# Kernel optimization log

Measured on AMD Instinct MI355X. Metric: run time of the kernel, lower is better.

The kernel has to match this reference:

```python
import jax, jax.numpy as jnp
import numpy as np

R = 8          # n attention heads / input capsules (config_spin['r'])
U2 = 1024      # 2 * d_lstm
DA = 512       # d_a
SC = 128       # n_seen_class
OA = 16        # output_atoms
NR = 3         # n_routing
B = 128
T = 256


def setup_inputs() -> dict:
    key = jax.random.key(0)
    k1, k2, k3, k4 = jax.random.split(key, 4)
    x = jax.random.normal(k1, (B, T, U2), jnp.float32)              # encoder output outp
    WS1 = jax.random.normal(k2, (R, DA, U2), jnp.float32) * 0.03    # r stacked Linear(2u->d_a) weights
    WS2 = jax.random.normal(k3, (R, U2, DA), jnp.float32) * 0.03    # r stacked Linear(d_a->2u) weights
    capsule_weights = jax.random.normal(k4, (R, U2, SC * OA), jnp.float32) * 0.03
    return {"x": x, "WS1": WS1, "WS2": WS2, "capsule_weights": capsule_weights}


def _squash(s):
    # s: [B, out_dim, atoms]; squash along atoms (dim=2 in torch)
    norm = jnp.linalg.norm(s, axis=2, keepdims=True)
    n2 = norm * norm
    return s / norm * (n2 / (1.0 + n2))


def reference(x, WS1, WS2, capsule_weights):
    # --- encoder_dim_att: r-head structured self-attention ---
    hbar = jax.nn.relu(jnp.einsum('btu,rau->brta', x, WS1))          # [B,r,T,d_a]
    scores = jnp.einsum('brta,rua->brtu', hbar, WS2)                 # [B,r,T,2u]
    alphas = jax.nn.softmax(scores, axis=2)                          # softmax over seq (torch dim=1)
    m = jnp.einsum('brtu,btu->bru', alphas, x)                       # sentence_embedding [B,r,2u]

    # --- votes: tiled multiply+sum == contraction over input_atoms ---
    votes = jnp.einsum('bru,ruo->bro', m, capsule_weights)           # [B,r,SC*OA]
    votes = votes.reshape(B, R, SC, OA)                              # [B,r,SC,OA]

    # --- dynamic routing ---
    logits0 = jnp.zeros((B, R, SC), x.dtype)

    def step(logits, _):
        route = jax.nn.softmax(logits, axis=2)                       # [B,r,SC]
        preact = jnp.einsum('brc,brco->bco', route, votes)           # [B,SC,OA]
        act = _squash(preact)                                        # [B,SC,OA]
        dist = jnp.einsum('brco,bco->brc', votes, act)               # agreement [B,r,SC]
        return logits + dist, act

    _, acts = jax.lax.scan(step, logits0, None, length=NR)
    activation = acts[-1]                                            # last-iteration activation
    return jnp.linalg.norm(activation, axis=-1)                      # class logits [B,SC]
```

## Files before the change

### kernel.cpp

```cpp
#include <hip/hip_runtime.h>


typedef __attribute__((ext_vector_type(8))) short bf16x8;
typedef __attribute__((ext_vector_type(8))) unsigned short u16x8;
typedef __attribute__((ext_vector_type(4))) float f32x4;

#define LDT 40

__device__ __forceinline__ unsigned short f2bf(float f) {
    unsigned u = __float_as_uint(f);
    u += 0x7FFF + ((u >> 16) & 1);
    return (unsigned short)(u >> 16);
}
__device__ __forceinline__ float bf2f(unsigned short h) {
    return __uint_as_float(((unsigned)h) << 16);
}

typedef __attribute__((address_space(1))) void gvoid;
typedef __attribute__((address_space(3))) void lvoid;
__device__ __forceinline__ void gll16(const unsigned short* g, unsigned short* l) {
    __builtin_amdgcn_global_load_lds((gvoid*)g, (lvoid*)l, 16, 0, 0);
}

__global__ __launch_bounds__(256) void k0_hi(const float* __restrict__ src,
                                             unsigned short* __restrict__ hi,
                                             int n4) {
    int i = blockIdx.x * 256 + threadIdx.x;
    if (i >= n4) return;
    float4 v = ((const float4*)src)[i];
    ushort4 h;
    h.x = f2bf(v.x); h.y = f2bf(v.y); h.z = f2bf(v.z); h.w = f2bf(v.w);
    ((ushort4*)hi)[i] = h;
}

__global__ __launch_bounds__(256) void k0_tsplit(const float* __restrict__ cw,
                                                 unsigned short* __restrict__ ch,
                                                 unsigned short* __restrict__ cl) {
    __shared__ unsigned short Th[64 * 68], Tl[64 * 68];
    const int tid = threadIdx.x;
    const int n0 = blockIdx.x * 64, k0 = blockIdx.y * 64, r = blockIdx.z;
    const float* src = cw + (size_t)r * 1024 * 2048;
#pragma unroll
    for (int p = 0; p < 4; p++) {
        const int kl = p * 16 + (tid >> 4);
        const int nl = (tid & 15) * 4;
        float4 v = *(const float4*)(src + (size_t)(k0 + kl) * 2048 + n0 + nl);
        float vv[4] = {v.x, v.y, v.z, v.w};
#pragma unroll
        for (int e = 0; e < 4; e++) {
            unsigned short h = f2bf(vv[e]);
            Th[(nl + e) * 68 + kl] = h;
            Tl[(nl + e) * 68 + kl] = f2bf(vv[e] - bf2f(h));
        }
    }
    __syncthreads();
    const int nl = tid >> 2, kl = (tid & 3) * 16;
    unsigned short* dh = ch + ((size_t)r * 2048 + n0 + nl) * 1024 + k0 + kl;
    unsigned short* dl = cl + ((size_t)r * 2048 + n0 + nl) * 1024 + k0 + kl;
    *(u16x8*)(dh)     = *(const u16x8*)&Th[nl * 68 + kl];
    *(u16x8*)(dh + 8) = *(const u16x8*)&Th[nl * 68 + kl + 8];
    *(u16x8*)(dl)     = *(const u16x8*)&Tl[nl * 68 + kl];
    *(u16x8*)(dl + 8) = *(const u16x8*)&Tl[nl * 68 + kl + 8];
}

__global__ __launch_bounds__(256) void k1_all(
    const unsigned short* __restrict__ Xb,
    const unsigned short* __restrict__ W1h,
    unsigned short* __restrict__ HhA) {
    __shared__ __align__(16) unsigned short Ah[2][128 * 32];
    __shared__ __align__(16) unsigned short Bh[2][128 * 32];
    const int tid = threadIdx.x;
    const int m0 = blockIdx.x * 128, n0 = blockIdx.y * 128, r = blockIdx.z;
    const int wave = tid >> 6, lane = tid & 63;
    const int wm = (wave >> 1) * 64, wn = (wave & 1) * 64;
    const int lx = lane & 15, qd = lane >> 4;
    const int rl = lane >> 2, cl = (lane & 3) * 8;

    f32x4 acc[4][4];
#pragma unroll
    for (int i = 0; i < 4; i++)
#pragma unroll
        for (int j = 0; j < 4; j++) acc[i][j] = (f32x4){0.f, 0.f, 0.f, 0.f};

    const unsigned short* asrc = Xb + (size_t)(m0 + rl) * 1024 + cl;
    const unsigned short* bsrc =
        W1h + (size_t)r * 512 * 1024 + (size_t)(n0 + rl) * 1024 + cl;

#define K1_STAGE(AD, BD, KK)                                         \
    do {                                                             \
        _Pragma("unroll") for (int s = 0; s < 2; s++) {              \
            const int c = wave * 2 + s;                              \
            gll16(asrc + (size_t)c * 16 * 1024 + (KK), (AD) + c * 512); \
            gll16(bsrc + (size_t)c * 16 * 1024 + (KK), (BD) + c * 512); \
        }                                                            \
    } while (0)

    K1_STAGE(Ah[0], Bh[0], 0);
    __syncthreads();
    int p = 0;
    for (int t = 0; t < 32; ++t) {
        if (t < 31) K1_STAGE(Ah[p ^ 1], Bh[p ^ 1], (t + 1) * 32);
        const unsigned short* Ab = Ah[p];
        const unsigned short* Bb = Bh[p];
        bf16x8 fa[4], fb[4];
#pragma unroll
        for (int i = 0; i < 4; i++) {
            fa[i] = *(const bf16x8*)&Ab[(wm + 16 * i + lx) * 32 + 8 * qd];
            fb[i] = *(const bf16x8*)&Bb[(wn + 16 * i + lx) * 32 + 8 * qd];
        }
#pragma unroll
        for (int i = 0; i < 4; i++)
#pragma unroll
            for (int j = 0; j < 4; j++)
                acc[i][j] = __builtin_amdgcn_mfma_f32_16x16x32_bf16(fa[i], fb[j], acc[i][j], 0, 0, 0);
        __syncthreads();
        p ^= 1;
    }
#undef K1_STAGE

    unsigned short* Hh = HhA + (size_t)r * 8192 * 512;
#pragma unroll
    for (int i = 0; i < 4; i++)
#pragma unroll
        for (int j = 0; j < 4; j++) {
            const int col = n0 + wn + 16 * j + lx;
#pragma unroll
            for (int p2 = 0; p2 < 4; p2++) {
                const int row = m0 + wm + 16 * i + 4 * qd + p2;
                Hh[(size_t)row * 512 + col] = f2bf(fmaxf(acc[i][j][p2], 0.f));
            }
        }
}

template <int XBF>
__global__ __launch_bounds__(256) void k1_hbar_mfma(
    const void* __restrict__ Xv,
    const unsigned short* __restrict__ Wh,
    unsigned short* __restrict__ Hh) {
    __shared__ unsigned short Ah[128 * LDT];
    __shared__ unsigned short Bh[128 * LDT];
    const int tid = threadIdx.x;
    const int m0 = blockIdx.x * 128, n0 = blockIdx.y * 128;
    const int wave = tid >> 6, lane = tid & 63;
    const int wm = (wave >> 1) * 64, wn = (wave & 1) * 64;
    const int lx = lane & 15, qd = lane >> 4;
    const int srow = tid >> 1, scol = (tid & 1) * 16;

    f32x4 acc[4][4];
#pragma unroll
    for (int i = 0; i < 4; i++)
#pragma unroll
        for (int j = 0; j < 4; j++) acc[i][j] = (f32x4){0.f, 0.f, 0.f, 0.f};

    const unsigned short* whrow = Wh + (size_t)(n0 + srow) * 1024 + scol;
    unsigned short* ah = &Ah[srow * LDT + scol];
    unsigned short* bh = &Bh[srow * LDT + scol];

    for (int k0 = 0; k0 < 1024; k0 += 32) {
        if (XBF) {
            const unsigned short* xrow =
                (const unsigned short*)Xv + (size_t)(m0 + srow) * 1024 + scol;
            u16x8 a0 = *(const u16x8*)(xrow + k0);
            u16x8 a1 = *(const u16x8*)(xrow + k0 + 8);
            *(u16x8*)(ah) = a0; *(u16x8*)(ah + 8) = a1;
        } else {
            const float* xrow = (const float*)Xv + (size_t)(m0 + srow) * 1024 + scol;
            float4 v0 = *(const float4*)(xrow + k0);
            float4 v1 = *(const float4*)(xrow + k0 + 4);
            float4 v2 = *(const float4*)(xrow + k0 + 8);
            float4 v3 = *(const float4*)(xrow + k0 + 12);
            float vv[16] = {v0.x, v0.y, v0.z, v0.w, v1.x, v1.y, v1.z, v1.w,
                            v2.x, v2.y, v2.z, v2.w, v3.x, v3.y, v3.z, v3.w};
            u16x8 p0, p1;
#pragma unroll
            for (int e = 0; e < 8; e++) p0[e] = f2bf(vv[e]);
#pragma unroll
            for (int e = 0; e < 8; e++) p1[e] = f2bf(vv[8 + e]);
            *(u16x8*)(ah) = p0; *(u16x8*)(ah + 8) = p1;
        }
        u16x8 b0 = *(const u16x8*)(whrow + k0);
        u16x8 b1 = *(const u16x8*)(whrow + k0 + 8);
        *(u16x8*)(bh) = b0; *(u16x8*)(bh + 8) = b1;
        __syncthreads();

        bf16x8 fa[4], fb[4];
#pragma unroll
        for (int i = 0; i < 4; i++) {
            fa[i] = *(const bf16x8*)&Ah[(wm + 16 * i + lx) * LDT + 8 * qd];
            fb[i] = *(const bf16x8*)&Bh[(wn + 16 * i + lx) * LDT + 8 * qd];
        }
#pragma unroll
        for (int i = 0; i < 4; i++)
#pragma unroll
            for (int j = 0; j < 4; j++)
                acc[i][j] = __builtin_amdgcn_mfma_f32_16x16x32_bf16(fa[i], fb[j], acc[i][j], 0, 0, 0);
        __syncthreads();
    }

#pragma unroll
    for (int i = 0; i < 4; i++)
#pragma unroll
        for (int j = 0; j < 4; j++) {
            const int col = n0 + wn + 16 * j + lx;
#pragma unroll
            for (int p = 0; p < 4; p++) {
                const int row = m0 + wm + 16 * i + 4 * qd + p;
                Hh[(size_t)row * 512 + col] = f2bf(fmaxf(acc[i][j][p], 0.f));
            }
        }
}

__global__ __launch_bounds__(256) void k2_allr(
    const unsigned short* __restrict__ HhA,
    const unsigned short* __restrict__ W2h,
    const float* __restrict__ x, float* __restrict__ m_out, int b0) {
    __shared__ __align__(16) unsigned short Ah[2][256 * 32];
    __shared__ __align__(16) unsigned short Bh[2][64 * 32];
    __shared__ float mred[256], sred[256], pred[256];
    const int tid = threadIdx.x;
    const int b_local = blockIdx.x, b = b0 + b_local;
    const int u0 = blockIdx.y * 64;
    const int r_base = blockIdx.z * 4;
    const int wave = tid >> 6, lane = tid & 63;
    const int lx = lane & 15, qd = lane >> 4;
    const int rl = lane >> 2, cl = (lane & 3) * 8;
    const int ub = wave * 16 + rl;
    const int uperm = 4 * (ub & 15) + (ub >> 4);

    for (int rr = 0; rr < 4; ++rr) {
        const int r = r_base + rr;
        const unsigned short* asrc =
            HhA + (size_t)r * 8192 * 512 + (size_t)(b_local * 256 + rl) * 512 + cl;
        const unsigned short* bsrc =
            W2h + (size_t)r * 1024 * 512 + (size_t)(u0 + uperm) * 512 + cl;

        f32x4 acc[4][4];
#pragma unroll
        for (int i = 0; i < 4; i++)
#pragma unroll
            for (int j = 0; j < 4; j++) acc[i][j] = (f32x4){0.f, 0.f, 0.f, 0.f};

#define K2_STAGE(AD, BD, KK)                                            \
    do {                                                                \
        _Pragma("unroll") for (int s = 0; s < 4; s++) {                 \
            const int c = wave * 4 + s;                                 \
            gll16(asrc + (size_t)c * 16 * 512 + (KK), (AD) + c * 512);  \
        }                                                               \
        gll16(bsrc + (KK), (BD) + wave * 512);                          \
    } while (0)

        K2_STAGE(Ah[0], Bh[0], 0);
        __syncthreads();
        int p = 0;
        for (int t = 0; t < 16; ++t) {
            if (t < 15) K2_STAGE(Ah[p ^ 1], Bh[p ^ 1], (t + 1) * 32);
            const unsigned short* Ab = Ah[p];
            const unsigned short* Bb = Bh[p];
            bf16x8 fa[4], fb[4];
#pragma unroll
            for (int i = 0; i < 4; i++) {
                fa[i] = *(const bf16x8*)&Ab[(64 * wave + 16 * i + lx) * 32 + 8 * qd];
                fb[i] = *(const bf16x8*)&Bb[(16 * i + lx) * 32 + 8 * qd];
            }
#pragma unroll
            for (int i = 0; i < 4; i++)
#pragma unroll
                for (int j = 0; j < 4; j++)
                    acc[i][j] = __builtin_amdgcn_mfma_f32_16x16x32_bf16(fa[i], fb[j], acc[i][j], 0, 0, 0);
            __syncthreads();
            p ^= 1;
        }
#undef K2_STAGE

        float cm[4];
#pragma unroll
        for (int j = 0; j < 4; j++) {
            float mx = acc[0][j][0];
#pragma unroll
            for (int i = 0; i < 4; i++)
#pragma unroll
                for (int p2 = 0; p2 < 4; p2++) mx = fmaxf(mx, acc[i][j][p2]);
            mx = fmaxf(mx, __shfl_xor(mx, 16, 64));
            mx = fmaxf(mx, __shfl_xor(mx, 32, 64));
            if (qd == 0) mred[wave * 64 + 16 * j + lx] = mx;
        }
        __syncthreads();
#pragma unroll
        for (int j = 0; j < 4; j++) {
            const int c = 16 * j + lx;
            cm[j] = fmaxf(fmaxf(mred[c], mred[64 + c]),
                          fmaxf(mred[128 + c], mred[192 + c]));
        }

        float ds[4] = {0.f, 0.f, 0.f, 0.f}, pm[4] = {0.f, 0.f, 0.f, 0.f};
        const float* xb = x + (size_t)b * 256 * 1024 + u0 + 4 * lx;
#pragma unroll
        for (int i = 0; i < 4; i++) {
#pragma unroll
            for (int p2 = 0; p2 < 4; p2++) {
                const int t = 64 * wave + 16 * i + 4 * qd + p2;
                float4 xv = *(const float4*)(xb + (size_t)t * 1024);
                float xa[4] = {xv.x, xv.y, xv.z, xv.w};
#pragma unroll
                for (int j = 0; j < 4; j++) {
                    float e = __expf(acc[i][j][p2] - cm[j]);
                    ds[j] += e;
                    pm[j] += e * xa[j];
                }
            }
        }
#pragma unroll
        for (int j = 0; j < 4; j++) {
            ds[j] += __shfl_xor(ds[j], 16, 64);
            ds[j] += __shfl_xor(ds[j], 32, 64);
            pm[j] += __shfl_xor(pm[j], 16, 64);
            pm[j] += __shfl_xor(pm[j], 32, 64);
            if (qd == 0) {
                sred[wave * 64 + 16 * j + lx] = ds[j];
                pred[wave * 64 + 16 * j + lx] = pm[j];
            }
        }
        __syncthreads();
        if (tid < 64) {
            float dsum = sred[tid] + sred[64 + tid] + sred[128 + tid] + sred[192 + tid];
            float psum = pred[tid] + pred[64 + tid] + pred[128 + tid] + pred[192 + tid];
            const int u = u0 + 4 * (tid & 15) + (tid >> 4);
            m_out[(size_t)(r * 128 + b) * 1024 + u] = psum / dsum;
        }
        __syncthreads();
    }
}

__global__ __launch_bounds__(256) void k2_mfma(
    const unsigned short* __restrict__ Hh,
    const unsigned short* __restrict__ W2h,
    const float* __restrict__ x, float* __restrict__ m_out, int b0, int r) {
    __shared__ __align__(16) unsigned short Ah[256 * 32];
    __shared__ __align__(16) unsigned short Bh[64 * 32];
    __shared__ float mred[256], sred[256], pred[256];
    const int tid = threadIdx.x;
    const int b_local = blockIdx.x, b = b0 + b_local;
    const int u0 = blockIdx.y * 64;
    const int wave = tid >> 6, lane = tid & 63;
    const int lx = lane & 15, qd = lane >> 4;
    const int rl = lane >> 2, cl = (lane & 3) * 8;

    f32x4 acc[4][4];
#pragma unroll
    for (int i = 0; i < 4; i++)
#pragma unroll
        for (int j = 0; j < 4; j++) acc[i][j] = (f32x4){0.f, 0.f, 0.f, 0.f};

    const unsigned short* asrc = Hh + (size_t)(b_local * 256 + rl) * 512 + cl;
    const int ub = wave * 16 + rl;
    const unsigned short* bsrc =
        W2h + (size_t)(u0 + 4 * (ub & 15) + (ub >> 4)) * 512 + cl;

    for (int k0 = 0; k0 < 512; k0 += 32) {
#pragma unroll
        for (int s = 0; s < 4; s++) {
            const int c = wave * 4 + s;
            gll16(asrc + (size_t)c * 16 * 512 + k0, &Ah[c * 512]);
        }
        gll16(bsrc + k0, &Bh[wave * 512]);
        __syncthreads();
        bf16x8 fa[4], fb[4];
#pragma unroll
        for (int i = 0; i < 4; i++) {
            fa[i] = *(const bf16x8*)&Ah[(64 * wave + 16 * i + lx) * 32 + 8 * qd];
            fb[i] = *(const bf16x8*)&Bh[(16 * i + lx) * 32 + 8 * qd];
        }
#pragma unroll
        for (int i = 0; i < 4; i++)
#pragma unroll
            for (int j = 0; j < 4; j++)
                acc[i][j] = __builtin_amdgcn_mfma_f32_16x16x32_bf16(fa[i], fb[j], acc[i][j], 0, 0, 0);
        __syncthreads();
    }

    float cm[4];
#pragma unroll
    for (int j = 0; j < 4; j++) {
        float mx = acc[0][j][0];
#pragma unroll
        for (int i = 0; i < 4; i++)
#pragma unroll
            for (int p = 0; p < 4; p++) mx = fmaxf(mx, acc[i][j][p]);
        mx = fmaxf(mx, __shfl_xor(mx, 16, 64));
        mx = fmaxf(mx, __shfl_xor(mx, 32, 64));
        if (qd == 0) mred[wave * 64 + 16 * j + lx] = mx;
    }
    __syncthreads();
#pragma unroll
    for (int j = 0; j < 4; j++) {
        const int c = 16 * j + lx;
        cm[j] = fmaxf(fmaxf(mred[c], mred[64 + c]), fmaxf(mred[128 + c], mred[192 + c]));
    }

    float ds[4] = {0.f, 0.f, 0.f, 0.f}, pm[4] = {0.f, 0.f, 0.f, 0.f};
    const float* xb = x + (size_t)b * 256 * 1024 + u0 + 4 * lx;
#pragma unroll
    for (int i = 0; i < 4; i++) {
#pragma unroll
        for (int p = 0; p < 4; p++) {
            const int t = 64 * wave + 16 * i + 4 * qd + p;
            float4 xv = *(const float4*)(xb + (size_t)t * 1024);
            float xa[4] = {xv.x, xv.y, xv.z, xv.w};
#pragma unroll
            for (int j = 0; j < 4; j++) {
                float e = __expf(acc[i][j][p] - cm[j]);
                ds[j] += e;
                pm[j] += e * xa[j];
            }
        }
    }
#pragma unroll
    for (int j = 0; j < 4; j++) {
        ds[j] += __shfl_xor(ds[j], 16, 64);
        ds[j] += __shfl_xor(ds[j], 32, 64);
        pm[j] += __shfl_xor(pm[j], 16, 64);
        pm[j] += __shfl_xor(pm[j], 32, 64);
        if (qd == 0) {
            sred[wave * 64 + 16 * j + lx] = ds[j];
            pred[wave * 64 + 16 * j + lx] = pm[j];
        }
    }
    __syncthreads();
    if (tid < 64) {
        float dsum = sred[tid] + sred[64 + tid] + sred[128 + tid] + sred[192 + tid];
        float psum = pred[tid] + pred[64 + tid] + pred[128 + tid] + pred[192 + tid];
        const int u = u0 + 4 * (tid & 15) + (tid >> 4);
        m_out[(size_t)(r * 128 + b) * 1024 + u] = psum / dsum;
    }
}

__global__ __launch_bounds__(256) void k3_votes_mfma(
    const float* __restrict__ Mb,
    const unsigned short* __restrict__ CWh,
    const unsigned short* __restrict__ CWl,
    float* __restrict__ V) {
    __shared__ unsigned short Ah[128 * LDT];
    __shared__ unsigned short Bh[64 * LDT], Bl[64 * LDT];
    const int tid = threadIdx.x;
    const int r = blockIdx.x, n0 = blockIdx.y * 64;
    const int wave = tid >> 6, lane = tid & 63;
    const int wr = wave >> 1, wc = wave & 1;
    const int lx = lane & 15, qd = lane >> 4;
    const int srow = tid >> 1, scol = (tid & 1) * 16;
    const int brow = tid >> 2, bcol = (tid & 3) * 8;

    const float* arow = Mb + (size_t)(r * 128 + srow) * 1024 + scol;
    const unsigned short* bhrow = CWh + ((size_t)r * 2048 + n0 + brow) * 1024 + bcol;
    const unsigned short* blrow = CWl + ((size_t)r * 2048 + n0 + brow) * 1024 + bcol;

    f32x4 acc[4][2];
#pragma unroll
    for (int i = 0; i < 4; i++)
#pragma unroll
        for (int j = 0; j < 2; j++) acc[i][j] = (f32x4){0.f, 0.f, 0.f, 0.f};

    for (int k0 = 0; k0 < 1024; k0 += 32) {
        float4 v0 = *(const float4*)(arow + k0);
        float4 v1 = *(const float4*)(arow + k0 + 4);
        float4 v2 = *(const float4*)(arow + k0 + 8);
        float4 v3 = *(const float4*)(arow + k0 + 12);
        float vv[16] = {v0.x, v0.y, v0.z, v0.w, v1.x, v1.y, v1.z, v1.w,
                        v2.x, v2.y, v2.z, v2.w, v3.x, v3.y, v3.z, v3.w};
        u16x8 p0, p1;
#pragma unroll
        for (int e = 0; e < 8; e++) p0[e] = f2bf(vv[e]);
#pragma unroll
        for (int e = 0; e < 8; e++) p1[e] = f2bf(vv[8 + e]);
        *(u16x8*)&Ah[srow * LDT + scol] = p0;
        *(u16x8*)&Ah[srow * LDT + scol + 8] = p1;
        *(u16x8*)&Bh[brow * LDT + bcol] = *(const u16x8*)(bhrow + k0);
        *(u16x8*)&Bl[brow * LDT + bcol] = *(const u16x8*)(blrow + k0);
        __syncthreads();

        bf16x8 fa[4], fbh[2], fbl[2];
#pragma unroll
        for (int i = 0; i < 4; i++)
            fa[i] = *(const bf16x8*)&Ah[(64 * wr + 16 * i + lx) * LDT + 8 * qd];
#pragma unroll
        for (int j = 0; j < 2; j++) {
            fbh[j] = *(const bf16x8*)&Bh[(32 * wc + 16 * j + lx) * LDT + 8 * qd];
            fbl[j] = *(const bf16x8*)&Bl[(32 * wc + 16 * j + lx) * LDT + 8 * qd];
        }
#pragma unroll
        for (int i = 0; i < 4; i++)
#pragma unroll
            for (int j = 0; j < 2; j++)
                acc[i][j] = __builtin_amdgcn_mfma_f32_16x16x32_bf16(fa[i], fbh[j], acc[i][j], 0, 0, 0);
#pragma unroll
        for (int i = 0; i < 4; i++)
#pragma unroll
            for (int j = 0; j < 2; j++)
                acc[i][j] = __builtin_amdgcn_mfma_f32_16x16x32_bf16(fa[i], fbl[j], acc[i][j], 0, 0, 0);
        __syncthreads();
    }

#pragma unroll
    for (int i = 0; i < 4; i++)
#pragma unroll
        for (int j = 0; j < 2; j++) {
            const int col = n0 + 32 * wc + 16 * j + lx;
#pragma unroll
            for (int p = 0; p < 4; p++) {
                const int row = 64 * wr + 16 * i + 4 * qd + p;
                V[((size_t)r * 128 + row) * 2048 + col] = acc[i][j][p];
            }
        }
}

__global__ __launch_bounds__(256) void k3_votes(const float* __restrict__ Mb,
                                                const float* __restrict__ CW,
                                                float* __restrict__ V) {
    __shared__ float As[16][132];
    __shared__ float Bs[16][132];
    const int tid = threadIdx.x;
    const int r = blockIdx.z;
    const int n0 = blockIdx.x * 128;
    const float* A = Mb + (size_t)r * 128 * 1024;
    const float* Bm = CW + (size_t)r * 1024 * 2048;
    float* C = V + (size_t)r * 128 * 2048;
    const int ty = tid >> 4, tx = tid & 15;
    const int k4 = (tid & 3) * 4, row = tid >> 2;
    const int n4 = (tid & 31) * 4, krow = tid >> 5;

    float acc[8][8];
#pragma unroll
    for (int i = 0; i < 8; i++)
#pragma unroll
        for (int j = 0; j < 8; j++) acc[i][j] = 0.f;

    for (int k0 = 0; k0 < 1024; k0 += 16) {
#pragma unroll
        for (int rr = 0; rr < 2; rr++) {
            const int m = row + rr * 64;
            float4 av = *(const float4*)(A + (size_t)m * 1024 + k0 + k4);
            As[k4 + 0][m] = av.x; As[k4 + 1][m] = av.y;
            As[k4 + 2][m] = av.z; As[k4 + 3][m] = av.w;
            const int k = krow + rr * 8;
            float4 bv = *(const float4*)(Bm + (size_t)(k0 + k) * 2048 + n0 + n4);
            *(float4*)(&Bs[k][n4]) = bv;
        }
        __syncthreads();
#pragma unroll
        for (int k = 0; k < 16; k++) {
            float a[8], b[8];
            *(float4*)(a)     = *(const float4*)(&As[k][ty * 8]);
            *(float4*)(a + 4) = *(const float4*)(&As[k][ty * 8 + 4]);
            *(float4*)(b)     = *(const float4*)(&Bs[k][tx * 8]);
            *(float4*)(b + 4) = *(const float4*)(&Bs[k][tx * 8 + 4]);
#pragma unroll
            for (int i = 0; i < 8; i++)
#pragma unroll
                for (int j = 0; j < 8; j++) acc[i][j] += a[i] * b[j];
        }
        __syncthreads();
    }
#pragma unroll
    for (int i = 0; i < 8; i++) {
        const int m = ty * 8 + i;
#pragma unroll
        for (int j = 0; j < 8; j += 4) {
            float4 v;
            v.x = acc[i][j + 0]; v.y = acc[i][j + 1];
            v.z = acc[i][j + 2]; v.w = acc[i][j + 3];
            *(float4*)(C + (size_t)m * 2048 + n0 + tx * 8 + j) = v;
        }
    }
}

__global__ __launch_bounds__(256) void k4_routing(const float* __restrict__ V,
                                                  float* __restrict__ out) {
    __shared__ float logits[8 * 128];
    __shared__ float route[8 * 128];
    __shared__ float preact[128 * 16];
    __shared__ float act[128 * 16];
    __shared__ float fred[128];
    const int b = blockIdx.x, tid = threadIdx.x;
    const float* vb = V + (size_t)b * 2048;

    for (int i = tid; i < 1024; i += 256) logits[i] = 0.f;
    __syncthreads();

    for (int it = 0; it < 3; it++) {
        {
            const int r = tid >> 5, g = tid & 31;
            float l[4];
#pragma unroll
            for (int q = 0; q < 4; q++) l[q] = logits[r * 128 + g + q * 32];
            float mx = fmaxf(fmaxf(l[0], l[1]), fmaxf(l[2], l[3]));
            for (int msk = 16; msk; msk >>= 1) mx = fmaxf(mx, __shfl_xor(mx, msk, 32));
            float e[4], s = 0.f;
#pragma unroll
            for (int q = 0; q < 4; q++) { e[q] = expf(l[q] - mx); s += e[q]; }
            for (int msk = 16; msk; msk >>= 1) s += __shfl_xor(s, msk, 32);
            float inv = 1.f / s;
#pragma unroll
            for (int q = 0; q < 4; q++) route[r * 128 + g + q * 32] = e[q] * inv;
        }
        __syncthreads();
        for (int i = tid; i < 2048; i += 256) {
            const int c = i >> 4;
            float a = 0.f;
#pragma unroll
            for (int r = 0; r < 8; r++)
                a += route[r * 128 + c] * vb[(size_t)r * 128 * 2048 + i];
            preact[i] = a;
        }
        __syncthreads();
        if (tid < 128) {
            float n2 = 0.f;
#pragma unroll
            for (int o = 0; o < 16; o++) { float p = preact[tid * 16 + o]; n2 += p * p; }
            fred[tid] = sqrtf(n2) / (1.f + n2);
        }
        __syncthreads();
        for (int i = tid; i < 2048; i += 256) act[i] = preact[i] * fred[i >> 4];
        __syncthreads();
        for (int i = tid; i < 1024; i += 256) {
            const int r = i >> 7, c = i & 127;
            float d = 0.f;
#pragma unroll
            for (int o = 0; o < 16; o++)
                d += vb[(size_t)r * 128 * 2048 + c * 16 + o] * act[c * 16 + o];
            logits[i] += d;
        }
        __syncthreads();
    }
    if (tid < 128) {
        float n2 = 0.f;
#pragma unroll
        for (int o = 0; o < 16; o++) { float a = act[tid * 16 + o]; n2 += a * a; }
        out[(size_t)b * 128 + tid] = sqrtf(n2);
    }
}

extern "C" void kernel_launch(void* const* d_in, const int* in_sizes, int n_in,
                              void* d_out, int out_size, void* d_ws, size_t ws_size,
                              hipStream_t stream) {
    const float* x   = (const float*)d_in[0];
    const float* WS1 = (const float*)d_in[1];
    const float* WS2 = (const float*)d_in[2];
    const float* cw  = (const float*)d_in[3];
    float* out = (float*)d_out;

    char* ws = (char*)d_ws;
    float* m_buf = (float*)ws;
    float* votes = (float*)(ws + ((size_t)4 << 20));
    unsigned short* W1h = (unsigned short*)(ws + ((size_t)12 << 20));
    unsigned short* W2h = (unsigned short*)(ws + ((size_t)20 << 20));

    const bool use_cw  = ws_size >= ((size_t)124 << 20);
    const bool use_xbf = ws_size >= ((size_t)188 << 20);

    const int nW4 = (8 * 512 * 1024) / 4;
    k0_hi<<<dim3((nW4 + 255) / 256), dim3(256), 0, stream>>>(WS1, W1h, nW4);
    k0_hi<<<dim3((nW4 + 255) / 256), dim3(256), 0, stream>>>(WS2, W2h, nW4);

    if (use_xbf) {
        unsigned short* Xbf = (unsigned short*)(ws + ((size_t)28 << 20));
        unsigned short* HhA = (unsigned short*)(ws + ((size_t)92 << 20));
        unsigned short* CWh = (unsigned short*)(ws + ((size_t)92 << 20));
        unsigned short* CWl = (unsigned short*)(ws + ((size_t)124 << 20));

        const int nX4 = (128 * 256 * 1024) / 4;
        k0_hi<<<dim3((nX4 + 255) / 256), dim3(256), 0, stream>>>(x, Xbf, nX4);

        for (int b0 = 0; b0 < 128; b0 += 32) {
            k1_all<<<dim3(64, 4, 8), dim3(256), 0, stream>>>(
                Xbf + (size_t)b0 * 256 * 1024, W1h, HhA);
            k2_allr<<<dim3(32, 16, 2), dim3(256), 0, stream>>>(
                HhA, W2h, x, m_buf, b0);
        }
        k0_tsplit<<<dim3(32, 16, 8), dim3(256), 0, stream>>>(cw, CWh, CWl);
        k3_votes_mfma<<<dim3(8, 32), dim3(256), 0, stream>>>(m_buf, CWh, CWl, votes);
    } else {
        unsigned short* CWh = (unsigned short*)(ws + ((size_t)28 << 20));
        unsigned short* CWl = (unsigned short*)(ws + ((size_t)60 << 20));
        const size_t hh_off = use_cw ? ((size_t)92 << 20) : ((size_t)28 << 20);
        unsigned short* Hh = (unsigned short*)(ws + hh_off);

        int CB = 128;
        {
            const size_t perb = (size_t)256 << 10;
            if (ws_size < hh_off + 128 * perb) {
                size_t avail = (ws_size > hh_off) ? (ws_size - hh_off) : perb;
                CB = (int)(avail / perb);
                if (CB < 1) CB = 1;
                if (CB > 128) CB = 128;
            }
        }

        if (use_cw)
            k0_tsplit<<<dim3(32, 16, 8), dim3(256), 0, stream>>>(cw, CWh, CWl);

        for (int b0 = 0; b0 < 128; b0 += CB) {
            const int bc = (128 - b0 < CB) ? (128 - b0) : CB;
            for (int r = 0; r < 8; r++) {
                k1_hbar_mfma<0><<<dim3(bc * 2, 4), dim3(256), 0, stream>>>(
                    (const void*)(x + (size_t)b0 * 256 * 1024),
                    W1h + (size_t)r * 512 * 1024, Hh);
                k2_mfma<<<dim3(bc, 16), dim3(256), 0, stream>>>(
                    Hh, W2h + (size_t)r * 1024 * 512, x, m_buf, b0, r);
            }
        }
        if (use_cw)
            k3_votes_mfma<<<dim3(8, 32), dim3(256), 0, stream>>>(m_buf, CWh, CWl, votes);
        else
            k3_votes<<<dim3(16, 1, 8), dim3(256), 0, stream>>>(m_buf, cw, votes);
    }
    k4_routing<<<dim3(128), dim3(256), 0, stream>>>(votes, out);
}
```

Baseline: 1.233 ms.

## Pre-pack X, W1, W2 into MFMA fragment layout and load fragments directly

Adds conversion kernels that write X, WS1 and WS2 as bf16 in MFMA-fragment-major order. The two GEMM kernels then load operand fragments straight from global memory into registers with software double-buffering, with no LDS staging and no barriers in the K loop. k1 writes hbar back out in the same fragment layout so k2 can read it directly. This removes LDS traffic and syncs, but operands shared between waves are no longer reused through LDS and now depend on L1/L2 hits.

```diff
diff --git a/kernel.cpp b/kernel.cpp
--- a/kernel.cpp
+++ b/kernel.cpp
@@ -33,6 +33,52 @@
     ((ushort4*)hi)[i] = h;
 }
 
+__global__ __launch_bounds__(256) void k0_xfrag(const float* __restrict__ x,
+                                                unsigned short* __restrict__ Xf) {
+    const int tid = threadIdx.x;
+    const int tb = blockIdx.x;
+    const int kb = blockIdx.y * 4 + (tid >> 6);
+    const int lane = tid & 63, lx = lane & 15, qd = lane >> 4;
+    const float* src = x + (size_t)(tb * 16 + lx) * 1024 + kb * 32 + qd * 8;
+    float4 v0 = *(const float4*)(src);
+    float4 v1 = *(const float4*)(src + 4);
+    u16x8 o;
+    o[0] = f2bf(v0.x); o[1] = f2bf(v0.y); o[2] = f2bf(v0.z); o[3] = f2bf(v0.w);
+    o[4] = f2bf(v1.x); o[5] = f2bf(v1.y); o[6] = f2bf(v1.z); o[7] = f2bf(v1.w);
+    *(u16x8*)(Xf + ((size_t)(tb * 32 + kb) * 512) + lane * 8) = o;
+}
+
+__global__ __launch_bounds__(256) void k0_w1frag(const float* __restrict__ W1,
+                                                 unsigned short* __restrict__ Wf) {
+    const int tid = threadIdx.x;
+    const int nb = blockIdx.x, r = blockIdx.z;
+    const int kb = blockIdx.y * 4 + (tid >> 6);
+    const int lane = tid & 63, lx = lane & 15, qd = lane >> 4;
+    const float* src = W1 + (size_t)r * 512 * 1024 +
+                       (size_t)(nb * 16 + lx) * 1024 + kb * 32 + qd * 8;
+    float4 v0 = *(const float4*)(src);
+    float4 v1 = *(const float4*)(src + 4);
+    u16x8 o;
+    o[0] = f2bf(v0.x); o[1] = f2bf(v0.y); o[2] = f2bf(v0.z); o[3] = f2bf(v0.w);
+    o[4] = f2bf(v1.x); o[5] = f2bf(v1.y); o[6] = f2bf(v1.z); o[7] = f2bf(v1.w);
+    *(u16x8*)(Wf + ((size_t)((r * 32 + nb) * 32 + kb) * 512) + lane * 8) = o;
+}
+
+__global__ __launch_bounds__(256) void k0_w2frag(const float* __restrict__ W2,
+                                                 unsigned short* __restrict__ Wf) {
+    const int tid = threadIdx.x;
+    const int ub = blockIdx.x, kb = blockIdx.y, r = blockIdx.z;
+    const int j = tid >> 6, lane = tid & 63, lx = lane & 15, qd = lane >> 4;
+    const float* src = W2 + (size_t)r * 1024 * 512 +
+                       (size_t)(ub * 64 + 4 * lx + j) * 512 + kb * 32 + qd * 8;
+    float4 v0 = *(const float4*)(src);
+    float4 v1 = *(const float4*)(src + 4);
+    u16x8 o;
+    o[0] = f2bf(v0.x); o[1] = f2bf(v0.y); o[2] = f2bf(v0.z); o[3] = f2bf(v0.w);
+    o[4] = f2bf(v1.x); o[5] = f2bf(v1.y); o[6] = f2bf(v1.z); o[7] = f2bf(v1.w);
+    *(u16x8*)(Wf + ((size_t)(((r * 16 + ub) * 4 + j) * 16 + kb) * 512) + lane * 8) = o;
+}
+
 __global__ __launch_bounds__(256) void k0_tsplit(const float* __restrict__ cw,
                                                  unsigned short* __restrict__ ch,
                                                  unsigned short* __restrict__ cl) {
@@ -63,18 +109,18 @@
     *(u16x8*)(dl + 8) = *(const u16x8*)&Tl[nl * 68 + kl + 8];
 }
 
-__global__ __launch_bounds__(256) void k1_all(
-    const unsigned short* __restrict__ Xb,
-    const unsigned short* __restrict__ W1h,
-    unsigned short* __restrict__ HhA) {
-    __shared__ __align__(16) unsigned short Ah[2][128 * 32];
-    __shared__ __align__(16) unsigned short Bh[2][128 * 32];
-    const int tid = threadIdx.x;
-    const int m0 = blockIdx.x * 128, n0 = blockIdx.y * 128, r = blockIdx.z;
+#define LDF(P, OFF) (*(const bf16x8*)((P) + (OFF)))
+
+__global__ __launch_bounds__(256, 3) void k1_frag(
+    const unsigned short* __restrict__ Xf,
+    const unsigned short* __restrict__ W1f,
+    unsigned short* __restrict__ HfA) {
+    const int tid = threadIdx.x;
+    const int bx = blockIdx.x, n0 = blockIdx.y * 128, r = blockIdx.z;
     const int wave = tid >> 6, lane = tid & 63;
     const int wm = (wave >> 1) * 64, wn = (wave & 1) * 64;
     const int lx = lane & 15, qd = lane >> 4;
-    const int rl = lane >> 2, cl = (lane & 3) * 8;
+    const size_t l8 = (size_t)lane * 8;
 
     f32x4 acc[4][4];
 #pragma unroll
@@ -82,54 +128,168 @@
 #pragma unroll
         for (int j = 0; j < 4; j++) acc[i][j] = (f32x4){0.f, 0.f, 0.f, 0.f};
 
-    const unsigned short* asrc = Xb + (size_t)(m0 + rl) * 1024 + cl;
-    const unsigned short* bsrc =
-        W1h + (size_t)r * 512 * 1024 + (size_t)(n0 + rl) * 1024 + cl;
-
-#define K1_STAGE(AD, BD, KK)                                         \
-    do {                                                             \
-        _Pragma("unroll") for (int s = 0; s < 2; s++) {              \
-            const int c = wave * 2 + s;                              \
-            gll16(asrc + (size_t)c * 16 * 1024 + (KK), (AD) + c * 512); \
-            gll16(bsrc + (size_t)c * 16 * 1024 + (KK), (BD) + c * 512); \
-        }                                                            \
-    } while (0)
-
-    K1_STAGE(Ah[0], Bh[0], 0);
-    __syncthreads();
-    int p = 0;
-    for (int t = 0; t < 32; ++t) {
-        if (t < 31) K1_STAGE(Ah[p ^ 1], Bh[p ^ 1], (t + 1) * 32);
-        const unsigned short* Ab = Ah[p];
-        const unsigned short* Bb = Bh[p];
-        bf16x8 fa[4], fb[4];
+    const unsigned short* ab[4];
+    const unsigned short* bb[4];
+#pragma unroll
+    for (int i = 0; i < 4; i++) {
+        ab[i] = Xf + ((size_t)(bx * 8 + (wm >> 4) + i) * 32) * 512 + l8;
+        bb[i] = W1f + ((size_t)(r * 32 + ((n0 + wn) >> 4) + i) * 32) * 512 + l8;
+    }
+
+    bf16x8 fa0[4], fb0[4], fa1[4], fb1[4];
+#pragma unroll
+    for (int i = 0; i < 4; i++) { fa0[i] = LDF(ab[i], 0); fb0[i] = LDF(bb[i], 0); }
+    for (int t = 0; t < 32; t += 2) {
+#pragma unroll
+        for (int i = 0; i < 4; i++) { fa1[i] = LDF(ab[i], 512); fb1[i] = LDF(bb[i], 512); }
+#pragma unroll
+        for (int i = 0; i < 4; i++)
+#pragma unroll
+            for (int j = 0; j < 4; j++)
+                acc[i][j] = __builtin_amdgcn_mfma_f32_16x16x32_bf16(fa0[i], fb0[j], acc[i][j], 0, 0, 0);
+        if (t + 2 < 32) {
+#pragma unroll
+            for (int i = 0; i < 4; i++) {
+                ab[i] += 1024; bb[i] += 1024;
+                fa0[i] = LDF(ab[i], 0); fb0[i] = LDF(bb[i], 0);
+            }
+        }
+#pragma unroll
+        for (int i = 0; i < 4; i++)
+#pragma unroll
+            for (int j = 0; j < 4; j++)
+                acc[i][j] = __builtin_amdgcn_mfma_f32_16x16x32_bf16(fa1[i], fb1[j], acc[i][j], 0, 0, 0);
+    }
+
+    unsigned short* H = HfA + (size_t)r * 4194304;
+    const int tb0 = bx * 8 + (wm >> 4);
+    const int kb0 = (n0 + wn) >> 5;
+#pragma unroll
+    for (int i = 0; i < 4; i++)
+#pragma unroll
+        for (int j = 0; j < 4; j++) {
+            const int qd2 = 2 * (j & 1) + (lx >> 3);
+            const size_t base =
+                ((size_t)((tb0 + i) * 16 + kb0 + (j >> 1)) * 512) +
+                (qd2 * 16 + 4 * qd) * 8 + (lx & 7);
+#pragma unroll
+            for (int p = 0; p < 4; p++)
+                H[base + p * 8] = f2bf(fmaxf(acc[i][j][p], 0.f));
+        }
+}
+
+__global__ __launch_bounds__(256, 3) void k2_frag(
+    const unsigned short* __restrict__ Hf,
+    const unsigned short* __restrict__ W2f,
+    const float* __restrict__ x, float* __restrict__ m_out, int b0) {
+    __shared__ float mred[256], sred[256], pred[256];
+    const int tid = threadIdx.x;
+    const int b_local = blockIdx.x, b = b0 + b_local;
+    const int u0 = blockIdx.y * 64;
+    const int r_base = blockIdx.z * 4;
+    const int wave = tid >> 6, lane = tid & 63;
+    const int lx = lane & 15, qd = lane >> 4;
+    const size_t l8 = (size_t)lane * 8;
+
+    for (int rr = 0; rr < 4; ++rr) {
+        const int r = r_base + rr;
+        const unsigned short* ab[4];
+        const unsigned short* bb[4];
 #pragma unroll
         for (int i = 0; i < 4; i++) {
-            fa[i] = *(const bf16x8*)&Ab[(wm + 16 * i + lx) * 32 + 8 * qd];
-            fb[i] = *(const bf16x8*)&Bb[(wn + 16 * i + lx) * 32 + 8 * qd];
-        }
-#pragma unroll
-        for (int i = 0; i < 4; i++)
-#pragma unroll
-            for (int j = 0; j < 4; j++)
-                acc[i][j] = __builtin_amdgcn_mfma_f32_16x16x32_bf16(fa[i], fb[j], acc[i][j], 0, 0, 0);
-        __syncthreads();
-        p ^= 1;
-    }
-#undef K1_STAGE
-
-    unsigned short* Hh = HhA + (size_t)r * 8192 * 512;
-#pragma unroll
-    for (int i = 0; i < 4; i++)
+            ab[i] = Hf + (size_t)r * 4194304 +
+                    ((size_t)(b_local * 16 + wave * 4 + i) * 16) * 512 + l8;
+            bb[i] = W2f + ((size_t)(((r * 16 + blockIdx.y) * 4 + i) * 16)) * 512 + l8;
+        }
+
+        f32x4 acc[4][4];
+#pragma unroll
+        for (int i = 0; i < 4; i++)
+#pragma unroll
+            for (int j = 0; j < 4; j++) acc[i][j] = (f32x4){0.f, 0.f, 0.f, 0.f};
+
+        bf16x8 fa0[4], fb0[4], fa1[4], fb1[4];
+#pragma unroll
+        for (int i = 0; i < 4; i++) { fa0[i] = LDF(ab[i], 0); fb0[i] = LDF(bb[i], 0); }
+        for (int t = 0; t < 16; t += 2) {
+#pragma unroll
+            for (int i = 0; i < 4; i++) { fa1[i] = LDF(ab[i], 512); fb1[i] = LDF(bb[i], 512); }
+#pragma unroll
+            for (int i = 0; i < 4; i++)
+#pragma unroll
+                for (int j = 0; j < 4; j++)
+                    acc[i][j] = __builtin_amdgcn_mfma_f32_16x16x32_bf16(fa0[i], fb0[j], acc[i][j], 0, 0, 0);
+            if (t + 2 < 16) {
+#pragma unroll
+                for (int i = 0; i < 4; i++) {
+                    ab[i] += 1024; bb[i] += 1024;
+                    fa0[i] = LDF(ab[i], 0); fb0[i] = LDF(bb[i], 0);
+                }
+            }
+#pragma unroll
+            for (int i = 0; i < 4; i++)
+#pragma unroll
+                for (int j = 0; j < 4; j++)
+                    acc[i][j] = __builtin_amdgcn_mfma_f32_16x16x32_bf16(fa1[i], fb1[j], acc[i][j], 0, 0, 0);
+        }
+
+        float cm[4];
 #pragma unroll
         for (int j = 0; j < 4; j++) {
-            const int col = n0 + wn + 16 * j + lx;
+            float mx = acc[0][j][0];
+#pragma unroll
+            for (int i = 0; i < 4; i++)
+#pragma unroll
+                for (int p2 = 0; p2 < 4; p2++) mx = fmaxf(mx, acc[i][j][p2]);
+            mx = fmaxf(mx, __shfl_xor(mx, 16, 64));
+            mx = fmaxf(mx, __shfl_xor(mx, 32, 64));
+            if (qd == 0) mred[wave * 64 + 16 * j + lx] = mx;
+        }
+        __syncthreads();
+#pragma unroll
+        for (int j = 0; j < 4; j++) {
+            const int c = 16 * j + lx;
+            cm[j] = fmaxf(fmaxf(mred[c], mred[64 + c]),
+                          fmaxf(mred[128 + c], mred[192 + c]));
+        }
+
+        float ds[4] = {0.f, 0.f, 0.f, 0.f}, pm[4] = {0.f, 0.f, 0.f, 0.f};
+        const float* xb = x + (size_t)b * 256 * 1024 + u0 + 4 * lx;
+#pragma unroll
+        for (int i = 0; i < 4; i++) {
 #pragma unroll
             for (int p2 = 0; p2 < 4; p2++) {
-                const int row = m0 + wm + 16 * i + 4 * qd + p2;
-                Hh[(size_t)row * 512 + col] = f2bf(fmaxf(acc[i][j][p2], 0.f));
-            }
-        }
+                const int t = 64 * wave + 16 * i + 4 * qd + p2;
+                float4 xv = *(const float4*)(xb + (size_t)t * 1024);
+                float xa[4] = {xv.x, xv.y, xv.z, xv.w};
+#pragma unroll
+                for (int j = 0; j < 4; j++) {
+                    float e = __expf(acc[i][j][p2] - cm[j]);
+                    ds[j] += e;
+                    pm[j] += e * xa[j];
+                }
+            }
+        }
+#pragma unroll
+        for (int j = 0; j < 4; j++) {
+            ds[j] += __shfl_xor(ds[j], 16, 64);
+            ds[j] += __shfl_xor(ds[j], 32, 64);
+            pm[j] += __shfl_xor(pm[j], 16, 64);
+            pm[j] += __shfl_xor(pm[j], 32, 64);
+            if (qd == 0) {
+                sred[wave * 64 + 16 * j + lx] = ds[j];
+                pred[wave * 64 + 16 * j + lx] = pm[j];
+            }
+        }
+        __syncthreads();
+        if (tid < 64) {
+            float dsum = sred[tid] + sred[64 + tid] + sred[128 + tid] + sred[192 + tid];
+            float psum = pred[tid] + pred[64 + tid] + pred[128 + tid] + pred[192 + tid];
+            const int u = u0 + 4 * (tid & 15) + (tid >> 4);
+            m_out[(size_t)(r * 128 + b) * 1024 + u] = psum / dsum;
+        }
+        __syncthreads();
+    }
 }
 
 template <int XBF>
@@ -210,127 +370,6 @@
         }
 }
 
-__global__ __launch_bounds__(256) void k2_allr(
-    const unsigned short* __restrict__ HhA,
-    const unsigned short* __restrict__ W2h,
-    const float* __restrict__ x, float* __restrict__ m_out, int b0) {
-    __shared__ __align__(16) unsigned short Ah[2][256 * 32];
-    __shared__ __align__(16) unsigned short Bh[2][64 * 32];
-    __shared__ float mred[256], sred[256], pred[256];
-    const int tid = threadIdx.x;
-    const int b_local = blockIdx.x, b = b0 + b_local;
-    const int u0 = blockIdx.y * 64;
-    const int r_base = blockIdx.z * 4;
-    const int wave = tid >> 6, lane = tid & 63;
-    const int lx = lane & 15, qd = lane >> 4;
-    const int rl = lane >> 2, cl = (lane & 3) * 8;
-    const int ub = wave * 16 + rl;
-    const int uperm = 4 * (ub & 15) + (ub >> 4);
-
-    for (int rr = 0; rr < 4; ++rr) {
-        const int r = r_base + rr;
-        const unsigned short* asrc =
-            HhA + (size_t)r * 8192 * 512 + (size_t)(b_local * 256 + rl) * 512 + cl;
-        const unsigned short* bsrc =
-            W2h + (size_t)r * 1024 * 512 + (size_t)(u0 + uperm) * 512 + cl;
-
-        f32x4 acc[4][4];
-#pragma unroll
-        for (int i = 0; i < 4; i++)
-#pragma unroll
-            for (int j = 0; j < 4; j++) acc[i][j] = (f32x4){0.f, 0.f, 0.f, 0.f};
-
-#define K2_STAGE(AD, BD, KK)                                            \
-    do {                                                                \
-        _Pragma("unroll") for (int s = 0; s < 4; s++) {                 \
-            const int c = wave * 4 + s;                                 \
-            gll16(asrc + (size_t)c * 16 * 512 + (KK), (AD) + c * 512);  \
-        }                                                               \
-        gll16(bsrc + (KK), (BD) + wave * 512);                          \
-    } while (0)
-
-        K2_STAGE(Ah[0], Bh[0], 0);
-        __syncthreads();
-        int p = 0;
-        for (int t = 0; t < 16; ++t) {
-            if (t < 15) K2_STAGE(Ah[p ^ 1], Bh[p ^ 1], (t + 1) * 32);
-            const unsigned short* Ab = Ah[p];
-            const unsigned short* Bb = Bh[p];
-            bf16x8 fa[4], fb[4];
-#pragma unroll
-            for (int i = 0; i < 4; i++) {
-                fa[i] = *(const bf16x8*)&Ab[(64 * wave + 16 * i + lx) * 32 + 8 * qd];
-                fb[i] = *(const bf16x8*)&Bb[(16 * i + lx) * 32 + 8 * qd];
-            }
-#pragma unroll
-            for (int i = 0; i < 4; i++)
-#pragma unroll
-                for (int j = 0; j < 4; j++)
-                    acc[i][j] = __builtin_amdgcn_mfma_f32_16x16x32_bf16(fa[i], fb[j], acc[i][j], 0, 0, 0);
-            __syncthreads();
-            p ^= 1;
-        }
-#undef K2_STAGE
-
-        float cm[4];
-#pragma unroll
-        for (int j = 0; j < 4; j++) {
-            float mx = acc[0][j][0];
-#pragma unroll
-            for (int i = 0; i < 4; i++)
-#pragma unroll
-                for (int p2 = 0; p2 < 4; p2++) mx = fmaxf(mx, acc[i][j][p2]);
-            mx = fmaxf(mx, __shfl_xor(mx, 16, 64));
-            mx = fmaxf(mx, __shfl_xor(mx, 32, 64));
-            if (qd == 0) mred[wave * 64 + 16 * j + lx] = mx;
-        }
-        __syncthreads();
-#pragma unroll
-        for (int j = 0; j < 4; j++) {
-            const int c = 16 * j + lx;
-            cm[j] = fmaxf(fmaxf(mred[c], mred[64 + c]),
-                          fmaxf(mred[128 + c], mred[192 + c]));
-        }
-
-        float ds[4] = {0.f, 0.f, 0.f, 0.f}, pm[4] = {0.f, 0.f, 0.f, 0.f};
-        const float* xb = x + (size_t)b * 256 * 1024 + u0 + 4 * lx;
-#pragma unroll
-        for (int i = 0; i < 4; i++) {
-#pragma unroll
-            for (int p2 = 0; p2 < 4; p2++) {
-                const int t = 64 * wave + 16 * i + 4 * qd + p2;
-                float4 xv = *(const float4*)(xb + (size_t)t * 1024);
-                float xa[4] = {xv.x, xv.y, xv.z, xv.w};
-#pragma unroll
-                for (int j = 0; j < 4; j++) {
-                    float e = __expf(acc[i][j][p2] - cm[j]);
-                    ds[j] += e;
-                    pm[j] += e * xa[j];
-                }
-            }
-        }
-#pragma unroll
-        for (int j = 0; j < 4; j++) {
-            ds[j] += __shfl_xor(ds[j], 16, 64);
-            ds[j] += __shfl_xor(ds[j], 32, 64);
-            pm[j] += __shfl_xor(pm[j], 16, 64);
-            pm[j] += __shfl_xor(pm[j], 32, 64);
-            if (qd == 0) {
-                sred[wave * 64 + 16 * j + lx] = ds[j];
-                pred[wave * 64 + 16 * j + lx] = pm[j];
-            }
-        }
-        __syncthreads();
-        if (tid < 64) {
-            float dsum = sred[tid] + sred[64 + tid] + sred[128 + tid] + sred[192 + tid];
-            float psum = pred[tid] + pred[64 + tid] + pred[128 + tid] + pred[192 + tid];
-            const int u = u0 + 4 * (tid & 15) + (tid >> 4);
-            m_out[(size_t)(r * 128 + b) * 1024 + u] = psum / dsum;
-        }
-        __syncthreads();
-    }
-}
-
 __global__ __launch_bounds__(256) void k2_mfma(
     const unsigned short* __restrict__ Hh,
     const unsigned short* __restrict__ W2h,
@@ -650,38 +689,41 @@
     char* ws = (char*)d_ws;
     float* m_buf = (float*)ws;
     float* votes = (float*)(ws + ((size_t)4 << 20));
-    unsigned short* W1h = (unsigned short*)(ws + ((size_t)12 << 20));
-    unsigned short* W2h = (unsigned short*)(ws + ((size_t)20 << 20));
 
     const bool use_cw  = ws_size >= ((size_t)124 << 20);
-    const bool use_xbf = ws_size >= ((size_t)188 << 20);
-
-    const int nW4 = (8 * 512 * 1024) / 4;
-    k0_hi<<<dim3((nW4 + 255) / 256), dim3(256), 0, stream>>>(WS1, W1h, nW4);
-    k0_hi<<<dim3((nW4 + 255) / 256), dim3(256), 0, stream>>>(WS2, W2h, nW4);
-
-    if (use_xbf) {
-        unsigned short* Xbf = (unsigned short*)(ws + ((size_t)28 << 20));
-        unsigned short* HhA = (unsigned short*)(ws + ((size_t)92 << 20));
+    const bool use_big = ws_size >= ((size_t)188 << 20);
+
+    if (use_big) {
+        unsigned short* W1f = (unsigned short*)(ws + ((size_t)12 << 20));
+        unsigned short* W2f = (unsigned short*)(ws + ((size_t)20 << 20));
+        unsigned short* Xf  = (unsigned short*)(ws + ((size_t)28 << 20));
+        unsigned short* Hf  = (unsigned short*)(ws + ((size_t)92 << 20));
         unsigned short* CWh = (unsigned short*)(ws + ((size_t)92 << 20));
         unsigned short* CWl = (unsigned short*)(ws + ((size_t)124 << 20));
 
-        const int nX4 = (128 * 256 * 1024) / 4;
-        k0_hi<<<dim3((nX4 + 255) / 256), dim3(256), 0, stream>>>(x, Xbf, nX4);
+        k0_w1frag<<<dim3(32, 8, 8), dim3(256), 0, stream>>>(WS1, W1f);
+        k0_w2frag<<<dim3(16, 16, 8), dim3(256), 0, stream>>>(WS2, W2f);
+        k0_xfrag<<<dim3(2048, 8), dim3(256), 0, stream>>>(x, Xf);
 
         for (int b0 = 0; b0 < 128; b0 += 32) {
-            k1_all<<<dim3(64, 4, 8), dim3(256), 0, stream>>>(
-                Xbf + (size_t)b0 * 256 * 1024, W1h, HhA);
-            k2_allr<<<dim3(32, 16, 2), dim3(256), 0, stream>>>(
-                HhA, W2h, x, m_buf, b0);
+            k1_frag<<<dim3(64, 4, 8), dim3(256), 0, stream>>>(
+                Xf + (size_t)b0 * 256 * 1024, W1f, Hf);
+            k2_frag<<<dim3(32, 16, 2), dim3(256), 0, stream>>>(
+                Hf, W2f, x, m_buf, b0);
         }
         k0_tsplit<<<dim3(32, 16, 8), dim3(256), 0, stream>>>(cw, CWh, CWl);
         k3_votes_mfma<<<dim3(8, 32), dim3(256), 0, stream>>>(m_buf, CWh, CWl, votes);
     } else {
+        unsigned short* W1h = (unsigned short*)(ws + ((size_t)12 << 20));
+        unsigned short* W2h = (unsigned short*)(ws + ((size_t)20 << 20));
         unsigned short* CWh = (unsigned short*)(ws + ((size_t)28 << 20));
         unsigned short* CWl = (unsigned short*)(ws + ((size_t)60 << 20));
         const size_t hh_off = use_cw ? ((size_t)92 << 20) : ((size_t)28 << 20);
         unsigned short* Hh = (unsigned short*)(ws + hh_off);
+
+        const int nW4 = (8 * 512 * 1024) / 4;
+        k0_hi<<<dim3((nW4 + 255) / 256), dim3(256), 0, stream>>>(WS1, W1h, nW4);
+        k0_hi<<<dim3((nW4 + 255) / 256), dim3(256), 0, stream>>>(WS2, W2h, nW4);
 
         int CB = 128;
         {
```

After: 1.545 ms. 1.25x slower.
